# Performance work log

Measured on AMD Instinct MI355X. Metric: run time of the kernel, lower is better.

The kernel has to match this reference:

```python
import jax, jax.numpy as jnp
import numpy as np

D_MODEL = 1024
N_HEADS = 16
D_K = 64
D_V = 64
LN_EPS = 1e-5


def setup_inputs() -> dict:
    key = jax.random.key(0)
    ks = jax.random.split(key, 12)
    B, S = 2, 2048
    s_in = 1.0 / np.sqrt(D_MODEL)
    s_out = 1.0 / np.sqrt(N_HEADS * D_V)
    Q = jax.random.normal(ks[0], (B, S, D_MODEL), dtype=jnp.float32)
    K = jax.random.normal(ks[1], (B, S, D_MODEL), dtype=jnp.float32)
    V = jax.random.normal(ks[2], (B, S, D_MODEL), dtype=jnp.float32)
    attn_mask = jnp.zeros((B, S, S), dtype=bool)
    Wq = jax.random.normal(ks[3], (D_MODEL, N_HEADS * D_K), dtype=jnp.float32) * s_in
    bq = jnp.zeros((N_HEADS * D_K,), dtype=jnp.float32)
    Wk = jax.random.normal(ks[4], (D_MODEL, N_HEADS * D_K), dtype=jnp.float32) * s_in
    bk = jnp.zeros((N_HEADS * D_K,), dtype=jnp.float32)
    Wv = jax.random.normal(ks[5], (D_MODEL, N_HEADS * D_V), dtype=jnp.float32) * s_in
    bv = jnp.zeros((N_HEADS * D_V,), dtype=jnp.float32)
    Wo = jax.random.normal(ks[6], (N_HEADS * D_V, D_MODEL), dtype=jnp.float32) * s_out
    bo = jnp.zeros((D_MODEL,), dtype=jnp.float32)
    gamma = jnp.ones((D_MODEL,), dtype=jnp.float32)
    beta = jnp.zeros((D_MODEL,), dtype=jnp.float32)
    return {"Q": Q, "K": K, "V": V, "attn_mask": attn_mask,
            "Wq": Wq, "bq": bq, "Wk": Wk, "bk": bk, "Wv": Wv, "bv": bv,
            "Wo": Wo, "bo": bo, "gamma": gamma, "beta": beta}


def _layer_norm(x, gamma, beta):
    mu = jnp.mean(x, axis=-1, keepdims=True)
    var = jnp.mean(jnp.square(x - mu), axis=-1, keepdims=True)
    return (x - mu) * jax.lax.rsqrt(var + LN_EPS) * gamma + beta


def reference(Q, K, V, attn_mask, Wq, bq, Wk, bk, Wv, bv, Wo, bo, gamma, beta):
    B, S, _ = Q.shape
    # projections -> [B, H, S, d]
    Qs = (Q @ Wq + bq).reshape(B, S, N_HEADS, D_K).transpose(0, 2, 1, 3)
    Ks = (K @ Wk + bk).reshape(B, S, N_HEADS, D_K).transpose(0, 2, 1, 3)
    Vs = (V @ Wv + bv).reshape(B, S, N_HEADS, D_V).transpose(0, 2, 1, 3)
    # scores [B, H, Sq, Sk]
    scores = jnp.einsum("bhqd,bhkd->bhqk", Qs, Ks) / np.sqrt(D_K).astype(np.float32)
    scores = jnp.where(attn_mask[:, None, :, :], jnp.float32(-1e9), scores)
    attn = jax.nn.softmax(scores, axis=-1)
    context = jnp.einsum("bhqk,bhkd->bhqd", attn, Vs)
    context = context.transpose(0, 2, 1, 3).reshape(B, S, N_HEADS * D_V)
    output = context @ Wo + bo
    output = _layer_norm(output + Q, gamma, beta)
    return (output, attn)
```

## Files before the change

### kernel.cpp

```cpp
#include <hip/hip_runtime.h>
#include <hip/hip_bf16.h>

#define S_LEN 2048
#define NH 16
#define HD 64
#define DM 1024

typedef float f32x4 __attribute__((ext_vector_type(4)));
typedef unsigned u32x4 __attribute__((ext_vector_type(4)));
typedef unsigned u32x2 __attribute__((ext_vector_type(2)));
typedef __bf16 bf16x8 __attribute__((ext_vector_type(8)));

#define BAR() __builtin_amdgcn_s_barrier()
#define VMCNT(N) asm volatile("s_waitcnt vmcnt(" #N ")" ::: "memory")

__device__ __forceinline__ unsigned short f2bf(float f) {
  union { float f; unsigned u; } v; v.f = f;
  unsigned r = v.u + 0x7fffu + ((v.u >> 16) & 1u);
  return (unsigned short)(r >> 16);
}

__device__ __forceinline__ unsigned pack2bf(float lo, float hi) {
  return (unsigned)f2bf(lo) | ((unsigned)f2bf(hi) << 16);
}

__device__ __forceinline__ void load_lds16(const void* g, void* l) {
  __builtin_amdgcn_global_load_lds((const __attribute__((address_space(1))) void*)g,
                                   (__attribute__((address_space(3))) void*)l, 16, 0, 0);
}

__global__ __launch_bounds__(256) void prep_kernel(const float* __restrict__ Qi,
                                                   const float* __restrict__ Ki,
                                                   const float* __restrict__ Vi,
                                                   unsigned short* __restrict__ Qb,
                                                   unsigned short* __restrict__ Kb,
                                                   unsigned short* __restrict__ Vb,
                                                   const float* __restrict__ Wq,
                                                   const float* __restrict__ Wk,
                                                   const float* __restrict__ Wv,
                                                   const float* __restrict__ Wo,
                                                   unsigned short* __restrict__ Wtq,
                                                   unsigned short* __restrict__ Wtk,
                                                   unsigned short* __restrict__ Wtv,
                                                   unsigned short* __restrict__ Wto) {
  __shared__ float t[32][33];
  const int bid = blockIdx.x;
  if (bid < 12288) {
    int sel = bid >> 12;
    int i = (bid & 4095) * 256 + threadIdx.x;
    const float* in = sel == 0 ? Qi : (sel == 1 ? Ki : Vi);
    unsigned short* out = sel == 0 ? Qb : (sel == 1 ? Kb : Vb);
    float4 v = reinterpret_cast<const float4*>(in)[i];
    ushort4 o;
    o.x = f2bf(v.x); o.y = f2bf(v.y); o.z = f2bf(v.z); o.w = f2bf(v.w);
    reinterpret_cast<ushort4*>(out)[i] = o;
  } else {
    int r = bid - 12288;
    int wi = r >> 10, ti = r & 1023;
    const float* W = wi == 0 ? Wq : (wi == 1 ? Wk : (wi == 2 ? Wv : Wo));
    unsigned short* Wt = wi == 0 ? Wtq : (wi == 1 ? Wtk : (wi == 2 ? Wtv : Wto));
    int bx = (ti & 31) * 32;
    int by = (ti >> 5) * 32;
    int tx = threadIdx.x & 31, ty = threadIdx.x >> 5;
    for (int i = ty; i < 32; i += 8) t[i][tx] = W[(size_t)(by + i) * DM + bx + tx];
    __syncthreads();
    for (int i = ty; i < 32; i += 8) Wt[(size_t)(bx + i) * DM + by + tx] = f2bf(t[tx][i]);
  }
}

__global__ __launch_bounds__(256) void gemm_qkv(const unsigned short* __restrict__ Qb,
                                                const unsigned short* __restrict__ Kb,
                                                const unsigned short* __restrict__ Vb,
                                                const unsigned short* __restrict__ Wtq,
                                                const unsigned short* __restrict__ Wtk,
                                                const unsigned short* __restrict__ Wtv,
                                                const float* __restrict__ bq,
                                                const float* __restrict__ bk,
                                                const float* __restrict__ bv,
                                                unsigned short* __restrict__ Qhd,
                                                unsigned short* __restrict__ Khd,
                                                unsigned short* __restrict__ Vtd) {
  constexpr int K = 1024;
  __shared__ unsigned short Al[128 * 32];
  __shared__ unsigned short Bl[128 * 32];
  const int z = blockIdx.z;
  const unsigned short* A = z == 0 ? Qb : (z == 1 ? Kb : Vb);
  const unsigned short* Bt = z == 0 ? Wtq : (z == 1 ? Wtk : Wtv);
  const float* bias = z == 0 ? bq : (z == 1 ? bk : bv);
  unsigned short* C = z == 0 ? Qhd : (z == 1 ? Khd : Vtd);
  const int tid = threadIdx.x;
  const int w = tid >> 6, l = tid & 63;
  const int m0 = blockIdx.x * 128, n0 = blockIdx.y * 128;
  const int wr = (w >> 1) * 64, wc = (w & 1) * 64;
  const int lr = l & 15, lk = l >> 4;
  f32x4 acc[4][4] = {};
  for (int kt = 0; kt < K; kt += 32) {
#pragma unroll
    for (int i = 0; i < 2; ++i) {
      int seg = i * 256 + tid;
      int row = seg >> 2, ks = (seg & 3) * 8;
      load_lds16(A + (size_t)(m0 + row) * K + kt + ks, Al + seg * 8);
      load_lds16(Bt + (size_t)(n0 + row) * K + kt + ks, Bl + seg * 8);
    }
    __syncthreads();
    bf16x8 af[4], bfr[4];
#pragma unroll
    for (int t = 0; t < 4; ++t) af[t] = *(const bf16x8*)(Al + (wr + t * 16 + lr) * 32 + lk * 8);
#pragma unroll
    for (int t = 0; t < 4; ++t) bfr[t] = *(const bf16x8*)(Bl + (wc + t * 16 + lr) * 32 + lk * 8);
#pragma unroll
    for (int i = 0; i < 4; ++i)
#pragma unroll
      for (int j = 0; j < 4; ++j)
        acc[i][j] = __builtin_amdgcn_mfma_f32_16x16x32_bf16(af[i], bfr[j], acc[i][j], 0, 0, 0);
    __syncthreads();
  }
  const int drow = lk * 4, dcol = lr;
  if (z < 2) {
#pragma unroll
    for (int i = 0; i < 4; ++i)
#pragma unroll
      for (int j = 0; j < 4; ++j) {
        int n = n0 + wc + j * 16 + dcol;
        float bv_ = bias[n];
        int h = n >> 6, d = n & 63;
#pragma unroll
        for (int r = 0; r < 4; ++r) {
          int m = m0 + wr + i * 16 + drow + r;
          int b = m >> 11, s = m & 2047;
          C[((size_t)(b * NH + h) * S_LEN + s) * HD + d] = f2bf(acc[i][j][r] + bv_);
        }
      }
  } else {
#pragma unroll
    for (int i = 0; i < 4; ++i) {
      int m = m0 + wr + i * 16 + drow;
      int b = m >> 11, s = m & 2047;
#pragma unroll
      for (int j = 0; j < 4; ++j) {
        int n = n0 + wc + j * 16 + dcol;
        float bv_ = bias[n];
        int h = n >> 6, d = n & 63;
        ushort4 o;
        o.x = f2bf(acc[i][j][0] + bv_);
        o.y = f2bf(acc[i][j][1] + bv_);
        o.z = f2bf(acc[i][j][2] + bv_);
        o.w = f2bf(acc[i][j][3] + bv_);
        *reinterpret_cast<ushort4*>(C + ((size_t)(b * NH + h) * HD + d) * S_LEN + s) = o;
      }
    }
  }
}

__global__ __launch_bounds__(256) void gemm_out(const unsigned short* __restrict__ A,
                                                const unsigned short* __restrict__ Bt,
                                                const float* __restrict__ bias,
                                                float* __restrict__ C) {
  constexpr int K = 1024;
  constexpr int N = 1024;
  __shared__ unsigned short Al[128 * 32];
  __shared__ unsigned short Bl[64 * 32];
  const int tid = threadIdx.x;
  const int w = tid >> 6, l = tid & 63;
  const int m0 = blockIdx.x * 128, n0 = blockIdx.y * 64;
  const int wr = (w >> 1) * 64, wc = (w & 1) * 32;
  const int lr = l & 15, lk = l >> 4;
  f32x4 acc[4][2] = {};
  for (int kt = 0; kt < K; kt += 32) {
#pragma unroll
    for (int i = 0; i < 2; ++i) {
      int seg = i * 256 + tid;
      int row = seg >> 2, ks = (seg & 3) * 8;
      load_lds16(A + (size_t)(m0 + row) * K + kt + ks, Al + seg * 8);
    }
    {
      int row = tid >> 2, ks = (tid & 3) * 8;
      load_lds16(Bt + (size_t)(n0 + row) * K + kt + ks, Bl + tid * 8);
    }
    __syncthreads();
    bf16x8 af[4], bfr[2];
#pragma unroll
    for (int t = 0; t < 4; ++t) af[t] = *(const bf16x8*)(Al + (wr + t * 16 + lr) * 32 + lk * 8);
#pragma unroll
    for (int t = 0; t < 2; ++t) bfr[t] = *(const bf16x8*)(Bl + (wc + t * 16 + lr) * 32 + lk * 8);
#pragma unroll
    for (int i = 0; i < 4; ++i)
#pragma unroll
      for (int j = 0; j < 2; ++j)
        acc[i][j] = __builtin_amdgcn_mfma_f32_16x16x32_bf16(af[i], bfr[j], acc[i][j], 0, 0, 0);
    __syncthreads();
  }
  const int drow = lk * 4, dcol = lr;
#pragma unroll
  for (int i = 0; i < 4; ++i)
#pragma unroll
    for (int j = 0; j < 2; ++j) {
      int n = n0 + wc + j * 16 + dcol;
      float bv = bias[n];
#pragma unroll
      for (int r = 0; r < 4; ++r) {
        int m = m0 + wr + i * 16 + drow + r;
        C[(size_t)m * N + n] = acc[i][j][r] + bv;
      }
    }
}

#define STG_K(T, BASE)                                                         \
  {                                                                            \
    int s_ = tid;                                                              \
    int row_ = s_ >> 3, cb_ = (s_ & 7) * 16;                                   \
    load_lds16((const char*)Kbh + (size_t)((T) * 64 + row_) * 128 +            \
                   (cb_ ^ ((row_ & 7) << 4)),                                  \
               (BASE) + s_ * 16);                                              \
  }

#define STG_V(T, BASE)                                                         \
  {                                                                            \
    int s_ = tid;                                                              \
    int row_ = s_ >> 3, cb_ = (s_ & 7) * 16;                                   \
    load_lds16((const char*)Vbh + (size_t)row_ * 4096 + (T) * 128 +            \
                   (cb_ ^ ((row_ & 7) << 4)),                                  \
               (BASE) + s_ * 16);                                              \
  }

#define QKT4(KPTR)                                                             \
  _Pragma("unroll") for (int st = 0; st < 4; ++st) {                           \
    const char* rp = (KPTR) + (st * 16 + lr) * 128;                            \
    bf16x8 k0 = *(const bf16x8*)(rp + a0);                                     \
    bf16x8 k1 = *(const bf16x8*)(rp + (a0 ^ 64));                              \
    f32x4 a = {};                                                              \
    a = __builtin_amdgcn_mfma_f32_16x16x32_bf16(k0, qf0, a, 0, 0, 0);          \
    a = __builtin_amdgcn_mfma_f32_16x16x32_bf16(k1, qf1, a, 0, 0, 0);          \
    acc[st] = a;                                                               \
  }

#define MASKADJ4(T)                                                            \
  _Pragma("unroll") for (int st = 0; st < 4; ++st) {                           \
    uchar4 m4 = *(const uchar4*)(mrow + (T) * 64 + st * 16 + lk * 4);          \
    if (m4.x) acc[st][0] = -8e9f;                                              \
    if (m4.y) acc[st][1] = -8e9f;                                              \
    if (m4.z) acc[st][2] = -8e9f;                                              \
    if (m4.w) acc[st][3] = -8e9f;                                              \
  }

#define MASK_PREPASS()                                                         \
  unsigned maskbits = 0;                                                       \
  _Pragma("unroll") for (int g4 = 0; g4 < 4; ++g4) {                           \
    unsigned mm[8];                                                            \
    const char* mp = (const char*)mrow + g4 * 512 + lk * 16;                   \
    _Pragma("unroll") for (int q8 = 0; q8 < 8; ++q8) {                         \
      u32x4 v = __builtin_nontemporal_load((const u32x4*)(mp + q8 * 64));      \
      mm[q8] = v.x | v.y | v.z | v.w;                                          \
    }                                                                          \
    _Pragma("unroll") for (int q8 = 0; q8 < 8; ++q8)                           \
      if (__any(mm[q8] != 0)) maskbits |= 1u << (g4 * 8 + q8);                 \
  }

__global__ __launch_bounds__(512, 4) void attn_p1_kernel(const unsigned short* __restrict__ Qh,
                                                         const unsigned short* __restrict__ Kh,
                                                         const unsigned short* __restrict__ Vt,
                                                         const unsigned char* __restrict__ mask,
                                                         float* __restrict__ lsum_out,
                                                         unsigned* __restrict__ mbits_out,
                                                         unsigned short* __restrict__ ctx) {
  __shared__ char lds[81920];
  char* const ldsK = lds;
  char* const ldsV = lds + 24576;
  const int tid = threadIdx.x;
  const int w = tid >> 6, l = tid & 63;
  const int lr = l & 15, lk = l >> 4;
  const int L = blockIdx.x;
  const int g = L & 7, j = L >> 3;
  const int bh = g * 4 + (j & 3);
  const int qt = j >> 2;
  const int q0w = qt * 128 + w * 16;
  const int b = bh >> 4, h = bh & 15;
  const unsigned short* Qbh = Qh + (size_t)bh * S_LEN * HD;
  const unsigned short* Kbh = Kh + (size_t)bh * S_LEN * HD;
  const unsigned short* Vbh = Vt + (size_t)bh * HD * S_LEN;
  const unsigned char* mrow = mask + (size_t)b * S_LEN * S_LEN + (size_t)(q0w + lr) * S_LEN;

  bf16x8 qf0 = *(const bf16x8*)(Qbh + (q0w + lr) * HD + lk * 8);
  bf16x8 qf1 = *(const bf16x8*)(Qbh + (q0w + lr) * HD + 32 + lk * 8);
  const int sw = (lr & 7) << 4;
  const int a0 = (lk * 16) ^ sw;
  const float sc = 0.125f;

  MASK_PREPASS()
  if (l == 0) mbits_out[L * 8 + w] = maskbits;

  f32x4 acc[4];
  f32x4 cacc[4] = {};
  float tsum = 0.f;

  {
    int cur = 0, stg = 2;
    STG_K(0, ldsK)
    STG_V(0, ldsV)
    STG_K(1, ldsK + 8192)
    STG_V(1, ldsV + 8192)
    for (int t = 0; t < 32; ++t) {
      BAR();
      if (t < 30) {
        STG_K(t + 2, ldsK + stg * 8192)
        STG_V(t + 2, ldsV + stg * 8192)
      }
      if (t < 30) { VMCNT(4); }
      else if (t == 30) { VMCNT(2); }
      else { VMCNT(0); }
      BAR();
      const char* Kp = ldsK + cur * 8192;
      const char* Vp = ldsV + cur * 8192;
      QKT4(Kp)
      if (maskbits & (1u << t)) { MASKADJ4(t) }
      unsigned pk0[4], pk1[4];
#pragma unroll
      for (int st = 0; st < 4; ++st) {
        float p0 = __expf(acc[st][0] * sc);
        float p1 = __expf(acc[st][1] * sc);
        float p2 = __expf(acc[st][2] * sc);
        float p3 = __expf(acc[st][3] * sc);
        tsum += p0 + p1 + p2 + p3;
        pk0[st] = pack2bf(p0, p1);
        pk1[st] = pack2bf(p2, p3);
      }
      char* Pw = lds + 49152 + (w * 2 + (t & 1)) * 2048;
#pragma unroll
      for (int st = 0; st < 4; ++st) {
        u32x2 pv;
        pv.x = pk0[st];
        pv.y = pk1[st];
        *(u32x2*)(Pw + lr * 128 + ((st * 32 + lk * 8) ^ sw)) = pv;
      }
      asm volatile("s_waitcnt lgkmcnt(0)" ::: "memory");
      __builtin_amdgcn_sched_barrier(0);
#pragma unroll
      for (int c = 0; c < 2; ++c) {
        bf16x8 af = *(const bf16x8*)(Pw + lr * 128 + ((c * 64 + lk * 16) ^ sw));
        const int voff = (c * 64 + lk * 16) ^ sw;
#pragma unroll
        for (int dt = 0; dt < 4; ++dt) {
          bf16x8 vb = *(const bf16x8*)(Vp + (dt * 16 + lr) * 128 + voff);
          cacc[dt] = __builtin_amdgcn_mfma_f32_16x16x32_bf16(af, vb, cacc[dt], 0, 0, 0);
        }
      }
      cur = cur == 2 ? 0 : cur + 1;
      stg = stg == 2 ? 0 : stg + 1;
    }
  }
  tsum += __shfl_xor(tsum, 16, 64);
  tsum += __shfl_xor(tsum, 32, 64);
  const float linv = 1.0f / tsum;
  if (lk == 0) lsum_out[(size_t)bh * S_LEN + q0w + lr] = linv;

#pragma unroll
  for (int dt = 0; dt < 4; ++dt)
#pragma unroll
    for (int r = 0; r < 4; ++r)
      ctx[(size_t)(b * S_LEN + q0w + lk * 4 + r) * DM + h * HD + dt * 16 + lr] =
          f2bf(cacc[dt][r] * linv);
}

__global__ __launch_bounds__(512, 4) void attn_st_kernel(const unsigned short* __restrict__ Qh,
                                                         const unsigned short* __restrict__ Kh,
                                                         const unsigned char* __restrict__ mask,
                                                         const float* __restrict__ linv_in,
                                                         const unsigned* __restrict__ mbits_in,
                                                         float* __restrict__ attn_out) {
  __shared__ char Pl[8][8192];
  const int tid = threadIdx.x;
  const int w = tid >> 6, l = tid & 63;
  const int lr = l & 15, lk = l >> 4;
  const int L = blockIdx.x;
  const int g = L & 7, j = L >> 3;
  const int bh = g * 4 + (j & 3);
  const int qt = j >> 2;
  const int q0w = qt * 128 + w * 16;
  const int b = bh >> 4;
  const unsigned short* Qbh = Qh + (size_t)bh * S_LEN * HD;
  const unsigned short* Kbh = Kh + (size_t)bh * S_LEN * HD;
  const unsigned char* mrow = mask + (size_t)b * S_LEN * S_LEN + (size_t)(q0w + lr) * S_LEN;
  char* const abase = (char*)(attn_out + ((size_t)bh * S_LEN + q0w) * S_LEN);

  const unsigned maskbits = mbits_in[L * 8 + w];
  const float linv = linv_in[(size_t)bh * S_LEN + q0w + lr];
  bf16x8 qf0 = *(const bf16x8*)(Qbh + (q0w + lr) * HD + lk * 8);
  bf16x8 qf1 = *(const bf16x8*)(Qbh + (q0w + lr) * HD + 32 + lk * 8);
  const float sc = 0.125f;
  const int swp = lr << 4;

  char* const Pw = Pl[w];
  f32x4 acc[4];
  for (int tt = 0; tt < 16; ++tt) {
#pragma unroll
    for (int half = 0; half < 2; ++half) {
      const int t = tt * 2 + half;
      bf16x8 kf0[4], kf1[4];
#pragma unroll
      for (int st = 0; st < 4; ++st) {
        const unsigned short* kp = Kbh + (size_t)(t * 64 + st * 16 + lr) * HD + lk * 8;
        kf0[st] = *(const bf16x8*)kp;
        kf1[st] = *(const bf16x8*)(kp + 32);
      }
#pragma unroll
      for (int st = 0; st < 4; ++st) {
        f32x4 a = {};
        a = __builtin_amdgcn_mfma_f32_16x16x32_bf16(kf0[st], qf0, a, 0, 0, 0);
        a = __builtin_amdgcn_mfma_f32_16x16x32_bf16(kf1[st], qf1, a, 0, 0, 0);
        acc[st] = a;
      }
      if (maskbits & (1u << t)) { MASKADJ4(t) }
#pragma unroll
      for (int st = 0; st < 4; ++st) {
        f32x4 p;
        p.x = __expf(acc[st][0] * sc) * linv;
        p.y = __expf(acc[st][1] * sc) * linv;
        p.z = __expf(acc[st][2] * sc) * linv;
        p.w = __expf(acc[st][3] * sc) * linv;
        *(f32x4*)(Pw + lr * 512 + ((half * 256 + st * 64 + lk * 16) ^ swp)) = p;
      }
    }
    asm volatile("s_waitcnt lgkmcnt(0)" ::: "memory");
    __builtin_amdgcn_sched_barrier(0);
#pragma unroll
    for (int s = 0; s < 8; ++s) {
      const int row = s * 2 + (l >> 5);
      const int ch = (l & 31) * 16;
      f32x4 v = *(const f32x4*)(Pw + row * 512 + (ch ^ (row << 4)));
      __builtin_nontemporal_store(v, (f32x4*)(abase + (size_t)row * 8192 + tt * 512 + ch));
    }
  }
}

__global__ __launch_bounds__(256) void ln_kernel(const float* __restrict__ pre,
                                                 const float* __restrict__ Qin,
                                                 const float* __restrict__ gamma,
                                                 const float* __restrict__ beta,
                                                 float* __restrict__ out) {
  __shared__ float red[4];
  const int row = blockIdx.x;
  const int tid = threadIdx.x;
  const int wv = tid >> 6, l = tid & 63;
  const float4 a = reinterpret_cast<const float4*>(pre + (size_t)row * DM)[tid];
  const float4 q = reinterpret_cast<const float4*>(Qin + (size_t)row * DM)[tid];
  float x0 = a.x + q.x, x1 = a.y + q.y, x2 = a.z + q.z, x3 = a.w + q.w;
  float s = x0 + x1 + x2 + x3;
#pragma unroll
  for (int off = 32; off >= 1; off >>= 1) s += __shfl_xor(s, off, 64);
  if (l == 0) red[wv] = s;
  __syncthreads();
  float mean = (red[0] + red[1] + red[2] + red[3]) * (1.0f / 1024.0f);
  __syncthreads();
  float d0 = x0 - mean, d1 = x1 - mean, d2 = x2 - mean, d3 = x3 - mean;
  float s2 = d0 * d0 + d1 * d1 + d2 * d2 + d3 * d3;
#pragma unroll
  for (int off = 32; off >= 1; off >>= 1) s2 += __shfl_xor(s2, off, 64);
  if (l == 0) red[wv] = s2;
  __syncthreads();
  float var = (red[0] + red[1] + red[2] + red[3]) * (1.0f / 1024.0f);
  float rstd = rsqrtf(var + 1e-5f);
  const float4 g = reinterpret_cast<const float4*>(gamma)[tid];
  const float4 bt = reinterpret_cast<const float4*>(beta)[tid];
  float4 o;
  o.x = d0 * rstd * g.x + bt.x;
  o.y = d1 * rstd * g.y + bt.y;
  o.z = d2 * rstd * g.z + bt.z;
  o.w = d3 * rstd * g.w + bt.w;
  reinterpret_cast<float4*>(out + (size_t)row * DM)[tid] = o;
}

extern "C" void kernel_launch(void* const* d_in, const int* in_sizes, int n_in,
                              void* d_out, int out_size, void* d_ws, size_t ws_size,
                              hipStream_t stream) {
  const float* Qi = (const float*)d_in[0];
  const float* Ki = (const float*)d_in[1];
  const float* Vi = (const float*)d_in[2];
  const unsigned char* mask = (const unsigned char*)d_in[3];
  const float* Wq = (const float*)d_in[4];
  const float* bq = (const float*)d_in[5];
  const float* Wk = (const float*)d_in[6];
  const float* bk = (const float*)d_in[7];
  const float* Wv = (const float*)d_in[8];
  const float* bv = (const float*)d_in[9];
  const float* Wo = (const float*)d_in[10];
  const float* bo = (const float*)d_in[11];
  const float* gamma = (const float*)d_in[12];
  const float* beta = (const float*)d_in[13];

  char* ws = (char*)d_ws;
  unsigned short* Qb = (unsigned short*)(ws);
  unsigned short* Kb = Qb + 4194304;
  unsigned short* Vb = Qb + 2 * 4194304;
  unsigned short* Wtq = (unsigned short*)(ws + 25165824);
  unsigned short* Wtk = Wtq + 1048576;
  unsigned short* Wtv = Wtq + 2 * 1048576;
  unsigned short* Wto = Wtq + 3 * 1048576;
  unsigned short* Qhd = (unsigned short*)(ws + 33554432);
  unsigned short* Khd = (unsigned short*)(ws + 41943040);
  unsigned short* Vtd = (unsigned short*)(ws + 50331648);
  unsigned short* ctx = (unsigned short*)(ws);
  float* preLN = (float*)(ws + 8388608);
  float* linv = (float*)(ws + 25165824 + 2097152);
  unsigned* mbits = (unsigned*)(ws + 25165824 + 2097152 + 262144);

  float* out0 = (float*)d_out;
  float* attn = out0 + 4194304;

  prep_kernel<<<16384, 256, 0, stream>>>(Qi, Ki, Vi, Qb, Kb, Vb,
                                         Wq, Wk, Wv, Wo, Wtq, Wtk, Wtv, Wto);
  dim3 gqkv(32, 8, 3);
  gemm_qkv<<<gqkv, 256, 0, stream>>>(Qb, Kb, Vb, Wtq, Wtk, Wtv,
                                     bq, bk, bv, Qhd, Khd, Vtd);
  attn_p1_kernel<<<512, 512, 0, stream>>>(Qhd, Khd, Vtd, mask, linv, mbits, ctx);
  attn_st_kernel<<<512, 512, 0, stream>>>(Qhd, Khd, mask, linv, mbits, attn);
  dim3 gg(32, 16);
  gemm_out<<<gg, 256, 0, stream>>>(ctx, Wto, bo, preLN);
  ln_kernel<<<4096, 256, 0, stream>>>(preLN, Qi, gamma, beta, out0);
}
```

Measured before the change: 319.6 us.

## Fuse attention probability store pass into context kernel

Merges the second attention kernel, which recomputed QK^T and wrote normalized probabilities, into the tail of the first kernel. The mask bits and the inverse row sums now stay in registers instead of going through global memory. The LDS staging buffer is reused for the probability tiles after a barrier. This removes one kernel launch and its Q/mask-bit/linv reloads, but the fused kernel's per-block runtime grows and the QK^T recomputation still happens serially within each block.

```diff
diff --git a/kernel.cpp b/kernel.cpp
--- a/kernel.cpp
+++ b/kernel.cpp
@@ -256,13 +256,12 @@
       if (__any(mm[q8] != 0)) maskbits |= 1u << (g4 * 8 + q8);                 \
   }
 
-__global__ __launch_bounds__(512, 4) void attn_p1_kernel(const unsigned short* __restrict__ Qh,
-                                                         const unsigned short* __restrict__ Kh,
-                                                         const unsigned short* __restrict__ Vt,
-                                                         const unsigned char* __restrict__ mask,
-                                                         float* __restrict__ lsum_out,
-                                                         unsigned* __restrict__ mbits_out,
-                                                         unsigned short* __restrict__ ctx) {
+__global__ __launch_bounds__(512, 4) void attn_fused_kernel(const unsigned short* __restrict__ Qh,
+                                                            const unsigned short* __restrict__ Kh,
+                                                            const unsigned short* __restrict__ Vt,
+                                                            const unsigned char* __restrict__ mask,
+                                                            float* __restrict__ attn_out,
+                                                            unsigned short* __restrict__ ctx) {
   __shared__ char lds[81920];
   char* const ldsK = lds;
   char* const ldsV = lds + 24576;
@@ -279,6 +278,7 @@
   const unsigned short* Kbh = Kh + (size_t)bh * S_LEN * HD;
   const unsigned short* Vbh = Vt + (size_t)bh * HD * S_LEN;
   const unsigned char* mrow = mask + (size_t)b * S_LEN * S_LEN + (size_t)(q0w + lr) * S_LEN;
+  char* const abase = (char*)(attn_out + ((size_t)bh * S_LEN + q0w) * S_LEN);
 
   bf16x8 qf0 = *(const bf16x8*)(Qbh + (q0w + lr) * HD + lk * 8);
   bf16x8 qf1 = *(const bf16x8*)(Qbh + (q0w + lr) * HD + 32 + lk * 8);
@@ -287,7 +287,6 @@
   const float sc = 0.125f;
 
   MASK_PREPASS()
-  if (l == 0) mbits_out[L * 8 + w] = maskbits;
 
   f32x4 acc[4];
   f32x4 cacc[4] = {};
@@ -351,7 +350,6 @@
   tsum += __shfl_xor(tsum, 16, 64);
   tsum += __shfl_xor(tsum, 32, 64);
   const float linv = 1.0f / tsum;
-  if (lk == 0) lsum_out[(size_t)bh * S_LEN + q0w + lr] = linv;
 
 #pragma unroll
   for (int dt = 0; dt < 4; ++dt)
@@ -359,38 +357,10 @@
     for (int r = 0; r < 4; ++r)
       ctx[(size_t)(b * S_LEN + q0w + lk * 4 + r) * DM + h * HD + dt * 16 + lr] =
           f2bf(cacc[dt][r] * linv);
-}
-
-__global__ __launch_bounds__(512, 4) void attn_st_kernel(const unsigned short* __restrict__ Qh,
-                                                         const unsigned short* __restrict__ Kh,
-                                                         const unsigned char* __restrict__ mask,
-                                                         const float* __restrict__ linv_in,
-                                                         const unsigned* __restrict__ mbits_in,
-                                                         float* __restrict__ attn_out) {
-  __shared__ char Pl[8][8192];
-  const int tid = threadIdx.x;
-  const int w = tid >> 6, l = tid & 63;
-  const int lr = l & 15, lk = l >> 4;
-  const int L = blockIdx.x;
-  const int g = L & 7, j = L >> 3;
-  const int bh = g * 4 + (j & 3);
-  const int qt = j >> 2;
-  const int q0w = qt * 128 + w * 16;
-  const int b = bh >> 4;
-  const unsigned short* Qbh = Qh + (size_t)bh * S_LEN * HD;
-  const unsigned short* Kbh = Kh + (size_t)bh * S_LEN * HD;
-  const unsigned char* mrow = mask + (size_t)b * S_LEN * S_LEN + (size_t)(q0w + lr) * S_LEN;
-  char* const abase = (char*)(attn_out + ((size_t)bh * S_LEN + q0w) * S_LEN);
-
-  const unsigned maskbits = mbits_in[L * 8 + w];
-  const float linv = linv_in[(size_t)bh * S_LEN + q0w + lr];
-  bf16x8 qf0 = *(const bf16x8*)(Qbh + (q0w + lr) * HD + lk * 8);
-  bf16x8 qf1 = *(const bf16x8*)(Qbh + (q0w + lr) * HD + 32 + lk * 8);
-  const float sc = 0.125f;
+
+  BAR();
+  char* const Pw2 = lds + w * 8192;
   const int swp = lr << 4;
-
-  char* const Pw = Pl[w];
-  f32x4 acc[4];
   for (int tt = 0; tt < 16; ++tt) {
 #pragma unroll
     for (int half = 0; half < 2; ++half) {
@@ -417,7 +387,7 @@
         p.y = __expf(acc[st][1] * sc) * linv;
         p.z = __expf(acc[st][2] * sc) * linv;
         p.w = __expf(acc[st][3] * sc) * linv;
-        *(f32x4*)(Pw + lr * 512 + ((half * 256 + st * 64 + lk * 16) ^ swp)) = p;
+        *(f32x4*)(Pw2 + lr * 512 + ((half * 256 + st * 64 + lk * 16) ^ swp)) = p;
       }
     }
     asm volatile("s_waitcnt lgkmcnt(0)" ::: "memory");
@@ -426,7 +396,7 @@
     for (int s = 0; s < 8; ++s) {
       const int row = s * 2 + (l >> 5);
       const int ch = (l & 31) * 16;
-      f32x4 v = *(const f32x4*)(Pw + row * 512 + (ch ^ (row << 4)));
+      f32x4 v = *(const f32x4*)(Pw2 + row * 512 + (ch ^ (row << 4)));
       __builtin_nontemporal_store(v, (f32x4*)(abase + (size_t)row * 8192 + tt * 512 + ch));
     }
   }
@@ -500,8 +470,6 @@
   unsigned short* Vtd = (unsigned short*)(ws + 50331648);
   unsigned short* ctx = (unsigned short*)(ws);
   float* preLN = (float*)(ws + 8388608);
-  float* linv = (float*)(ws + 25165824 + 2097152);
-  unsigned* mbits = (unsigned*)(ws + 25165824 + 2097152 + 262144);
 
   float* out0 = (float*)d_out;
   float* attn = out0 + 4194304;
@@ -511,8 +479,7 @@
   dim3 gqkv(32, 8, 3);
   gemm_qkv<<<gqkv, 256, 0, stream>>>(Qb, Kb, Vb, Wtq, Wtk, Wtv,
                                      bq, bk, bv, Qhd, Khd, Vtd);
-  attn_p1_kernel<<<512, 512, 0, stream>>>(Qhd, Khd, Vtd, mask, linv, mbits, ctx);
-  attn_st_kernel<<<512, 512, 0, stream>>>(Qhd, Khd, mask, linv, mbits, attn);
+  attn_fused_kernel<<<512, 512, 0, stream>>>(Qhd, Khd, Vtd, mask, attn, ctx);
   dim3 gg(32, 16);
   gemm_out<<<gg, 256, 0, stream>>>(ctx, Wto, bo, preLN);
   ln_kernel<<<4096, 256, 0, stream>>>(preLN, Qi, gamma, beta, out0);
```

Result: faster. 300.5 us, median of 2 (-6.0%).
